# Optimization experiments

Hardware: AMD Instinct MI355X
Metric: run time of the kernel (lower is better)

Reference implementation:

```python
import jax, jax.numpy as jnp
import numpy as np

D_MODEL = 1024
N_HEADS = 16
ALPHA = 0.7
C_PARAM = 5
CUTOFF = C_PARAM // 2 + 1  # 3
LN_EPS = 1e-12
B, S = 4, 2048


def setup_inputs() -> dict:
    key = jax.random.key(0)
    ks = jax.random.split(key, 10)
    d = D_MODEL
    scale = 1.0 / np.sqrt(d)
    return {
        "input_tensor": jax.random.normal(ks[0], (B, S, d), dtype=jnp.float32),
        "attention_mask": jnp.ones((1, 1, S, S), dtype=jnp.int32),
        "sqrt_beta": jax.random.normal(ks[1], (1, 1, d), dtype=jnp.float32),
        "ln_gamma": jnp.ones((d,), dtype=jnp.float32),
        "ln_beta": jnp.zeros((d,), dtype=jnp.float32),
        "q_w": jax.random.normal(ks[2], (d, d), dtype=jnp.float32) * scale,
        "q_b": jnp.zeros((d,), dtype=jnp.float32),
        "k_w": jax.random.normal(ks[3], (d, d), dtype=jnp.float32) * scale,
        "k_b": jnp.zeros((d,), dtype=jnp.float32),
        "v_w": jax.random.normal(ks[4], (d, d), dtype=jnp.float32) * scale,
        "v_b": jnp.zeros((d,), dtype=jnp.float32),
    }


def _layer_norm(x, g, b):
    mu = jnp.mean(x, axis=-1, keepdims=True)
    var = jnp.mean(jnp.square(x - mu), axis=-1, keepdims=True)
    return (x - mu) * jax.lax.rsqrt(var + LN_EPS) * g + b


def bsarec_layer(x, mask, sqrt_beta, ln_gamma, ln_beta, q_w, q_b, k_w, k_b, v_w, v_b):
    batch, seq_len, hidden = x.shape
    # ---- FrequencyLayer (DSP branch) ----
    xf = jnp.fft.rfft(x, axis=1, norm='ortho')                 # [B, S//2+1, D]
    freq = jnp.arange(xf.shape[1])[None, :, None]
    low_pass = jnp.fft.irfft(jnp.where(freq < CUTOFF, xf, 0.0), n=seq_len, axis=1, norm='ortho')
    high_pass = x - low_pass
    seq_fft = low_pass + jnp.square(sqrt_beta) * high_pass
    dsp = _layer_norm(seq_fft + x, ln_gamma, ln_beta)          # dropout=0 -> identity
    # ---- MultiHeadAttention (GSP branch) ----
    h, d_k = N_HEADS, hidden // N_HEADS
    def split(t):  # [B,S,D] -> [B,H,S,d_k]
        return t.reshape(batch, seq_len, h, d_k).transpose(0, 2, 1, 3)
    q = split(x @ q_w.T + q_b)
    k = split(x @ k_w.T + k_b)
    v = split(x @ v_w.T + v_b)
    scores = jnp.einsum('bhsd,bhtd->bhst', q, k) / jnp.sqrt(jnp.float32(d_k))
    scores = jnp.where(mask == 0, -jnp.inf, scores)
    scores = scores - jnp.max(scores)                           # global max, as in source
    p = jax.nn.softmax(scores, axis=-1)
    p = jnp.where(jnp.isnan(p), 0.0, p)
    out = jnp.einsum('bhst,bhtd->bhsd', p, v)
    gsp = out.transpose(0, 2, 1, 3).reshape(batch, seq_len, hidden)
    return ALPHA * dsp + (1.0 - ALPHA) * gsp


def reference(input_tensor, attention_mask, sqrt_beta, ln_gamma, ln_beta, q_w, q_b, k_w, k_b, v_w, v_b):
    return bsarec_layer(input_tensor, attention_mask, sqrt_beta, ln_gamma, ln_beta,
                        q_w, q_b, k_w, k_b, v_w, v_b)
```

## Files before the change

### kernel.cpp

```cpp
#include <hip/hip_runtime.h>

#define S_LEN 2048
#define DM 1024
#define NB 4
#define NROWS (NB * S_LEN)
#define NHEADS 16
#define DK 64

typedef __bf16 bf16x8 __attribute__((ext_vector_type(8)));
typedef __bf16 bf16x2 __attribute__((ext_vector_type(2)));
typedef float f32x4 __attribute__((ext_vector_type(4)));
typedef float f32x2 __attribute__((ext_vector_type(2)));
typedef unsigned u32x4 __attribute__((ext_vector_type(4)));

struct __align__(8) us4 { unsigned short x, y, z, w; };

__device__ __forceinline__ unsigned cvt2(float a, float b) {
    f32x2 t; t.x = a; t.y = b;
    bf16x2 h = __builtin_convertvector(t, bf16x2);
    return __builtin_bit_cast(unsigned, h);
}
__device__ __forceinline__ unsigned short f2bf(float f) {
    __bf16 h = (__bf16)f;
    return __builtin_bit_cast(unsigned short, h);
}

__device__ __forceinline__ void gl2lds16(const void* g, void* l) {
    __builtin_amdgcn_global_load_lds(
        (const __attribute__((address_space(1))) unsigned int*)g,
        (__attribute__((address_space(3))) unsigned int*)l, 16, 0, 0);
}

#if __has_builtin(__builtin_amdgcn_exp2f)
#define EXP2F(x) __builtin_amdgcn_exp2f(x)
#else
#define EXP2F(x) exp2f(x)
#endif

__global__ __launch_bounds__(256) void prep(
    const float* __restrict__ x, float* __restrict__ coef,
    unsigned short* __restrict__ xbf, const float* __restrict__ qw,
    const float* __restrict__ kw, const float* __restrict__ vw,
    unsigned short* __restrict__ wbf) {
    int bx = blockIdx.x;
    if (bx >= 512) {
        int idx = ((bx - 512) * 256 + threadIdx.x) * 2;
        int which = idx >> 20, off = idx & 0xFFFFF;
        const float* src = (which == 0) ? qw : ((which == 1) ? kw : vw);
        float2 v = *(const float2*)(&src[off]);
        *(unsigned*)(&wbf[idx]) = cvt2(v.x, v.y);
        return;
    }
    int b = bx >> 7, dc = (bx >> 5) & 3, tc = bx & 31;
    int d = dc * 256 + threadIdx.x;
    __shared__ float tw[4][64];
    if (threadIdx.x < 64) {
        const float omega = 6.283185307179586476925f / (float)S_LEN;
        float sn, cs;
        __sincosf(omega * (float)(tc * 64 + threadIdx.x), &sn, &cs);
        tw[0][threadIdx.x] = sn;
        tw[1][threadIdx.x] = cs;
        tw[2][threadIdx.x] = 2.f * sn * cs;
        tw[3][threadIdx.x] = cs * cs - sn * sn;
    }
    __syncthreads();
    float c0 = 0.f, c1 = 0.f, s1 = 0.f, c2 = 0.f, s2 = 0.f;
    for (int i = 0; i < 64; ++i) {
        int t = tc * 64 + i;
        long idx = (long)(b * S_LEN + t) * DM + d;
        float v = x[idx];
        xbf[idx] = f2bf(v);
        c0 += v;
        c1 += v * tw[1][i];
        s1 += v * tw[0][i];
        c2 += v * tw[3][i];
        s2 += v * tw[2][i];
    }
    int base = b * DM + d;
    atomicAdd(&coef[0 * 4096 + base], c0);
    atomicAdd(&coef[1 * 4096 + base], c1);
    atomicAdd(&coef[2 * 4096 + base], s1);
    atomicAdd(&coef[3 * 4096 + base], c2);
    atomicAdd(&coef[4 * 4096 + base], s2);
}

__global__ __launch_bounds__(256) void dsp_ln(
    const float* __restrict__ x, const float* __restrict__ coef,
    const float* __restrict__ sqrt_beta, const float* __restrict__ gamma,
    const float* __restrict__ beta, const unsigned short* __restrict__ Og,
    float* __restrict__ out) {
    int row = blockIdx.x;
    int b = row >> 11, t = row & (S_LEN - 1);
    int tid = threadIdx.x, lane = tid & 63, wave = tid >> 6;
    const float omega = 6.283185307179586476925f / (float)S_LEN;
    float sn, cs;
    __sincosf(omega * (float)t, &sn, &cs);
    float c2t = cs * cs - sn * sn, s2t = 2.f * sn * cs;
    int d0 = tid * 4;
    long base = (long)row * DM;
    float4 xv = *(const float4*)(&x[base + d0]);
    int cb = b * DM + d0;
    float4 C0 = *(const float4*)(&coef[0 * 4096 + cb]);
    float4 C1 = *(const float4*)(&coef[1 * 4096 + cb]);
    float4 S1 = *(const float4*)(&coef[2 * 4096 + cb]);
    float4 C2 = *(const float4*)(&coef[3 * 4096 + cb]);
    float4 S2 = *(const float4*)(&coef[4 * 4096 + cb]);
    float4 sb = *(const float4*)(&sqrt_beta[d0]);
    const float inv_s = 1.0f / (float)S_LEN;
    float y[4];
#pragma unroll
    for (int i = 0; i < 4; ++i) {
        float c0 = (&C0.x)[i], c1 = (&C1.x)[i], s1 = (&S1.x)[i],
              c2 = (&C2.x)[i], s2 = (&S2.x)[i];
        float lp = (c0 + 2.f * (c1 * cs + s1 * sn) + 2.f * (c2 * c2t + s2 * s2t)) * inv_s;
        float xx = (&xv.x)[i];
        float b2 = (&sb.x)[i];
        b2 = b2 * b2;
        y[i] = xx + lp + b2 * (xx - lp);
    }
    float ssum = y[0] + y[1] + y[2] + y[3];
    float ssq = y[0] * y[0] + y[1] * y[1] + y[2] * y[2] + y[3] * y[3];
#pragma unroll
    for (int m = 1; m < 64; m <<= 1) {
        ssum += __shfl_xor(ssum, m, 64);
        ssq += __shfl_xor(ssq, m, 64);
    }
    __shared__ float red[8];
    if (lane == 0) { red[wave] = ssum; red[4 + wave] = ssq; }
    __syncthreads();
    float S = red[0] + red[1] + red[2] + red[3];
    float SQ = red[4] + red[5] + red[6] + red[7];
    float mu = S * (1.0f / DM);
    float var = SQ * (1.0f / DM) - mu * mu;
    float rstd = rsqrtf(var + 1e-12f);
    float4 g = *(const float4*)(&gamma[d0]);
    float4 be = *(const float4*)(&beta[d0]);
    us4 gv = *(const us4*)(&Og[((long)((b << 4) + (d0 >> 6)) * S_LEN + t) * DK + (d0 & 63)]);
    const unsigned short* gp = (const unsigned short*)&gv;
    float4 o;
#pragma unroll
    for (int i = 0; i < 4; ++i)
        (&o.x)[i] = 0.7f * ((y[i] - mu) * rstd * (&g.x)[i] + (&be.x)[i]) +
                    0.3f * __uint_as_float((unsigned)gp[i] << 16);
    *(float4*)(&out[base + d0]) = o;
}

__global__ __launch_bounds__(256) void gemm_qkv(
    const unsigned short* __restrict__ A, const unsigned short* __restrict__ W,
    const float* __restrict__ qb, const float* __restrict__ kb,
    const float* __restrict__ vb, unsigned short* __restrict__ Qo,
    unsigned short* __restrict__ Ko, unsigned short* __restrict__ Vt_g) {
    const int m0 = blockIdx.y * 128;
    const int n0g = blockIdx.x * 128;
    const int which = n0g >> 10;
    const int n0 = n0g & 1023;
    const int tid = threadIdx.x;
    const int lane = tid & 63, wave = tid >> 6;
    const int wm = wave >> 1, wn = wave & 1;
    const int r = lane & 15, q = lane >> 4;
    __shared__ __align__(16) unsigned short Sm[8192];
    unsigned short* As = Sm;
    unsigned short* Bs = Sm + 4096;
    const int lrow = lane >> 2;
    const int lch = (lane & 3) * 8;
    f32x4 acc[4][4] = {};
    for (int k0 = 0; k0 < DM; k0 += 32) {
        __syncthreads();
#pragma unroll
        for (int e = 0; e < 2; ++e) {
            int blk = e * 4 + wave;
            int row = blk * 16 + lrow;
            gl2lds16(&A[(long)(m0 + row) * DM + k0 + lch], &As[blk * 512 + lane * 8]);
            gl2lds16(&W[(long)(n0g + row) * DM + k0 + lch], &Bs[blk * 512 + lane * 8]);
        }
        __syncthreads();
        bf16x8 af[4], bfr[4];
#pragma unroll
        for (int i = 0; i < 4; ++i) {
            af[i] = *(const bf16x8*)(&As[(wm * 64 + i * 16 + r) * 32 + q * 8]);
            bfr[i] = *(const bf16x8*)(&Bs[(wn * 64 + i * 16 + r) * 32 + q * 8]);
        }
#pragma unroll
        for (int mi = 0; mi < 4; ++mi)
#pragma unroll
            for (int ni = 0; ni < 4; ++ni)
                acc[mi][ni] = __builtin_amdgcn_mfma_f32_16x16x32_bf16(
                    af[mi], bfr[ni], acc[mi][ni], 0, 0, 0);
    }
    const float* bias = (which == 0) ? qb : ((which == 1) ? kb : vb);
    if (which < 2) {
        const float qs = (which == 0) ? 0.18033688011112042f : 1.0f;
        unsigned short* Out = (which == 0) ? Qo : Ko;
#pragma unroll
        for (int p = 0; p < 4; ++p) {
            __syncthreads();
            if (wm == (p >> 1)) {
#pragma unroll
                for (int mi2 = 0; mi2 < 2; ++mi2) {
                    int mi = (p & 1) * 2 + mi2;
                    int rowL = mi2 * 16 + q * 4;
#pragma unroll
                    for (int ni = 0; ni < 4; ++ni) {
                        int col = wn * 64 + ni * 16 + r;
                        float bv = bias[n0 + col];
#pragma unroll
                        for (int reg = 0; reg < 4; ++reg)
                            Sm[(rowL + reg) * 134 + col] = f2bf((acc[mi][ni][reg] + bv) * qs);
                    }
                }
            }
            __syncthreads();
            int rowL = wave * 8 + (lane >> 3);
            int cc = (lane & 7) * 16;
            uint4 w0 = *(const uint4*)(&Sm[rowL * 134 + cc]);
            uint4 w1 = *(const uint4*)(&Sm[rowL * 134 + cc + 8]);
            long gb = (long)(m0 + p * 32 + rowL) * DM + n0 + cc;
            *(uint4*)(&Out[gb]) = w0;
            *(uint4*)(&Out[gb + 8]) = w1;
        }
    } else {
        const int bb = m0 >> 11, sg = m0 & (S_LEN - 1);
#pragma unroll
        for (int p = 0; p < 4; ++p) {
            __syncthreads();
            if (wn == (p >> 1)) {
#pragma unroll
                for (int ni2 = 0; ni2 < 2; ++ni2) {
                    int ni = (p & 1) * 2 + ni2;
                    int colL = ni2 * 16 + r;
                    float bv = bias[n0 + p * 32 + colL];
#pragma unroll
                    for (int mi = 0; mi < 4; ++mi) {
                        int s = wm * 64 + mi * 16 + q * 4;
                        *(unsigned*)(&Sm[colL * 134 + s]) =
                            cvt2(acc[mi][ni][0] + bv, acc[mi][ni][1] + bv);
                        *(unsigned*)(&Sm[colL * 134 + s + 2]) =
                            cvt2(acc[mi][ni][2] + bv, acc[mi][ni][3] + bv);
                    }
                }
            }
            __syncthreads();
            int colL = wave * 8 + (lane >> 3);
            int sc = (lane & 7) * 16;
            uint4 w0 = *(const uint4*)(&Sm[colL * 134 + sc]);
            uint4 w1 = *(const uint4*)(&Sm[colL * 134 + sc + 8]);
            long gb = ((long)bb * DM + n0 + p * 32 + colL) * S_LEN + sg + sc;
            *(uint4*)(&Vt_g[gb]) = w0;
            *(uint4*)(&Vt_g[gb + 8]) = w1;
        }
    }
}

__global__ __launch_bounds__(256, 3) void attn(
    const unsigned short* __restrict__ Q, const unsigned short* __restrict__ K,
    const unsigned short* __restrict__ Vt_g, unsigned short* __restrict__ Og) {
    int bx = blockIdx.x;
    int bh = bx & 63, qt = bx >> 6;
    int b = bh >> 4, h = bh & 15;
    const int tid = threadIdx.x, lane = tid & 63, wave = tid >> 6;
    const int r = lane & 15, q = lane >> 4;
    const int hc = h * DK;
    const int q0 = qt * 128 + wave * 32;

    bf16x8 aq[2][2];
#pragma unroll
    for (int mt = 0; mt < 2; ++mt) {
        long rowQ = (long)(b * S_LEN + q0 + mt * 16 + r) * DM + hc;
        aq[mt][0] = *(const bf16x8*)(&Q[rowQ + q * 8]);
        aq[mt][1] = *(const bf16x8*)(&Q[rowQ + 32 + q * 8]);
    }

    __shared__ __align__(16) unsigned short Ks[2][4096];
    __shared__ __align__(16) unsigned short Vt[2][4096];
    __shared__ float denL[128];

    f32x4 accO[2][4] = {};
    float den[2] = {};

    const int lr = lane >> 3, lc = lane & 7;
    const int cw0 = wave * 2, cw1 = cw0 + 1;
    const int ld0 = cw0 * 512, ld1 = cw1 * 512;
    const int row0 = cw0 * 8 + lr, row1 = cw1 * 8 + lr;
    const int cg0 = lc ^ lr;
    const int cg1 = lc ^ lr ^ 4;
    const unsigned short* kp0 = K + (long)(b * S_LEN + row0) * DM + hc + cg0 * 8;
    const unsigned short* kp1 = K + (long)(b * S_LEN + row1) * DM + hc + cg1 * 8;
    const unsigned short* vp0 = Vt_g + (long)(bh * 64 + row0) * S_LEN + cg0 * 8;
    const unsigned short* vp1 = Vt_g + (long)(bh * 64 + row1) * S_LEN + cg1 * 8;

    const int lo = r & 3, hi = r >> 2;
    const int abase = (hi * 8 + lo) * 64;
    const int ca = (q ^ lo ^ ((hi & 1) << 2)) * 8;
    const int cb2 = ca ^ 32;
    const int va0 = (q ^ (r & 7) ^ (((r >> 3) & 1) << 2)) * 8;
    const int va1 = va0 ^ 32;

    gl2lds16(kp0, &Ks[0][ld0 + lane * 8]);
    gl2lds16(kp1, &Ks[0][ld1 + lane * 8]);
    gl2lds16(vp0, &Vt[0][ld0 + lane * 8]);
    gl2lds16(vp1, &Vt[0][ld1 + lane * 8]);
    kp0 += 64 * DM; kp1 += 64 * DM; vp0 += 64; vp1 += 64;
    asm volatile("s_waitcnt vmcnt(0)" ::: "memory");
    __builtin_amdgcn_s_barrier();

    for (int t = 0; t < 32; ++t) {
        const int cur = t & 1;
        if (t < 31) {
            const int nb = cur ^ 1;
            gl2lds16(kp0, &Ks[nb][ld0 + lane * 8]);
            gl2lds16(kp1, &Ks[nb][ld1 + lane * 8]);
            gl2lds16(vp0, &Vt[nb][ld0 + lane * 8]);
            gl2lds16(vp1, &Vt[nb][ld1 + lane * 8]);
            kp0 += 64 * DM; kp1 += 64 * DM; vp0 += 64; vp1 += 64;
        }
        const unsigned short* Kc = Ks[cur];
        const unsigned short* Vc = Vt[cur];
#pragma unroll
        for (int c = 0; c < 2; ++c) {
            const int cb64 = c * 2048;
            bf16x8 ak00 = *(const bf16x8*)(&Kc[cb64 + abase + ca]);
            bf16x8 ak01 = *(const bf16x8*)(&Kc[cb64 + abase + cb2]);
            bf16x8 ak10 = *(const bf16x8*)(&Kc[cb64 + 256 + abase + cb2]);
            bf16x8 ak11 = *(const bf16x8*)(&Kc[cb64 + 256 + abase + ca]);
            const int va = c ? va1 : va0;
            bf16x8 bv[4];
            bv[0] = *(const bf16x8*)(&Vc[(0 * 16 + r) * 64 + va]);
            bv[1] = *(const bf16x8*)(&Vc[(1 * 16 + r) * 64 + va]);
            bv[2] = *(const bf16x8*)(&Vc[(2 * 16 + r) * 64 + va]);
            bv[3] = *(const bf16x8*)(&Vc[(3 * 16 + r) * 64 + va]);
#pragma unroll
            for (int mt = 0; mt < 2; ++mt) {
                f32x4 sa = {}, sb = {};
                sa = __builtin_amdgcn_mfma_f32_16x16x32_bf16(ak00, aq[mt][0], sa, 0, 0, 0);
                sa = __builtin_amdgcn_mfma_f32_16x16x32_bf16(ak01, aq[mt][1], sa, 0, 0, 0);
                sb = __builtin_amdgcn_mfma_f32_16x16x32_bf16(ak10, aq[mt][0], sb, 0, 0, 0);
                sb = __builtin_amdgcn_mfma_f32_16x16x32_bf16(ak11, aq[mt][1], sb, 0, 0, 0);
                float p0 = EXP2F(sa[0]), p1 = EXP2F(sa[1]);
                float p2 = EXP2F(sa[2]), p3 = EXP2F(sa[3]);
                float p4 = EXP2F(sb[0]), p5 = EXP2F(sb[1]);
                float p6 = EXP2F(sb[2]), p7 = EXP2F(sb[3]);
                den[mt] += ((p0 + p1) + (p2 + p3)) + ((p4 + p5) + (p6 + p7));
                u32x4 wv;
                wv.x = cvt2(p0, p1); wv.y = cvt2(p2, p3);
                wv.z = cvt2(p4, p5); wv.w = cvt2(p6, p7);
                bf16x8 ap = __builtin_bit_cast(bf16x8, wv);
#pragma unroll
                for (int dt = 0; dt < 4; ++dt)
                    accO[mt][dt] = __builtin_amdgcn_mfma_f32_16x16x32_bf16(
                        ap, bv[dt], accO[mt][dt], 0, 0, 0);
            }
        }
        asm volatile("s_waitcnt vmcnt(0)" ::: "memory");
        __builtin_amdgcn_s_barrier();
    }
#pragma unroll
    for (int mt = 0; mt < 2; ++mt) {
        float d = den[mt];
        d += __shfl_xor(d, 16, 64);
        d += __shfl_xor(d, 32, 64);
        if (q == 0) denL[wave * 32 + mt * 16 + r] = d;
    }
#pragma unroll
    for (int mt = 0; mt < 2; ++mt) {
        float4 dv = *(const float4*)(&denL[wave * 32 + mt * 16 + q * 4]);
        float rs[4];
#pragma unroll
        for (int reg = 0; reg < 4; ++reg) rs[reg] = 1.0f / (&dv.x)[reg];
        long obase = (long)bh * S_LEN + q0 + mt * 16 + q * 4;
#pragma unroll
        for (int dt = 0; dt < 4; ++dt) {
            int col = dt * 16 + r;
#pragma unroll
            for (int reg = 0; reg < 4; ++reg)
                Og[(obase + reg) * DK + col] = f2bf(accO[mt][dt][reg] * rs[reg]);
        }
    }
}

extern "C" void kernel_launch(void* const* d_in, const int* in_sizes, int n_in,
                              void* d_out, int out_size, void* d_ws, size_t ws_size,
                              hipStream_t stream) {
    const float* x = (const float*)d_in[0];
    const float* sqrt_beta = (const float*)d_in[2];
    const float* gamma = (const float*)d_in[3];
    const float* beta = (const float*)d_in[4];
    const float* qw = (const float*)d_in[5];
    const float* qb = (const float*)d_in[6];
    const float* kw = (const float*)d_in[7];
    const float* kb = (const float*)d_in[8];
    const float* vw = (const float*)d_in[9];
    const float* vb = (const float*)d_in[10];
    float* out = (float*)d_out;

    char* ws = (char*)d_ws;
    float* coef = (float*)ws;
    unsigned short* xbf = (unsigned short*)(ws + 81920);
    unsigned short* wbf = (unsigned short*)(ws + 81920 + 16777216);
    unsigned short* Qb = (unsigned short*)(ws + 81920 + 16777216 + 6291456);
    unsigned short* Kb = Qb + (long)NROWS * DM;
    unsigned short* Vt_g = Kb + (long)NROWS * DM;
    unsigned short* Og = xbf;

    hipMemsetAsync(coef, 0, 5 * 4096 * sizeof(float), stream);
    prep<<<6656, 256, 0, stream>>>(x, coef, xbf, qw, kw, vw, wbf);
    dim3 ggrid(3 * DM / 128, NROWS / 128);
    gemm_qkv<<<ggrid, 256, 0, stream>>>(xbf, wbf, qb, kb, vb, Qb, Kb, Vt_g);
    attn<<<NB * NHEADS * (S_LEN / 128), 256, 0, stream>>>(Qb, Kb, Vt_g, Og);
    dsp_ln<<<NROWS, 256, 0, stream>>>(x, coef, sqrt_beta, gamma, beta, Og, out);
}
```

Before: 300.3 us.

## Triple-buffer K/V tiles in attention and raise priority around MFMA section

Turns the K/V shared-memory staging in the attention kernel from double to triple buffering. Two tiles are prefetched ahead and the loop waits with vmcnt(4) instead of vmcnt(0), so one tile load can stay in flight across the barrier. It also raises wave priority with s_setprio during the MFMA compute section. LDS use per block grows from about 32KB to 48KB, which may lower occupancy.

```diff
diff --git a/kernel.cpp b/kernel.cpp
--- a/kernel.cpp
+++ b/kernel.cpp
@@ -270,8 +270,8 @@
         aq[mt][1] = *(const bf16x8*)(&Q[rowQ + 32 + q * 8]);
     }
 
-    __shared__ __align__(16) unsigned short Ks[2][4096];
-    __shared__ __align__(16) unsigned short Vt[2][4096];
+    __shared__ __align__(16) unsigned short Ks[3][4096];
+    __shared__ __align__(16) unsigned short Vt[3][4096];
     __shared__ float denL[128];
 
     f32x4 accO[2][4] = {};
@@ -295,26 +295,29 @@
     const int va0 = (q ^ (r & 7) ^ (((r >> 3) & 1) << 2)) * 8;
     const int va1 = va0 ^ 32;
 
-    gl2lds16(kp0, &Ks[0][ld0 + lane * 8]);
-    gl2lds16(kp1, &Ks[0][ld1 + lane * 8]);
-    gl2lds16(vp0, &Vt[0][ld0 + lane * 8]);
-    gl2lds16(vp1, &Vt[0][ld1 + lane * 8]);
-    kp0 += 64 * DM; kp1 += 64 * DM; vp0 += 64; vp1 += 64;
-    asm volatile("s_waitcnt vmcnt(0)" ::: "memory");
+#define STAGE(buf)                                    \
+    do {                                              \
+        gl2lds16(kp0, &Ks[buf][ld0 + lane * 8]);      \
+        gl2lds16(kp1, &Ks[buf][ld1 + lane * 8]);      \
+        gl2lds16(vp0, &Vt[buf][ld0 + lane * 8]);      \
+        gl2lds16(vp1, &Vt[buf][ld1 + lane * 8]);      \
+        kp0 += 64 * DM; kp1 += 64 * DM; vp0 += 64; vp1 += 64; \
+    } while (0)
+
+    STAGE(0);
+    STAGE(1);
+    asm volatile("s_waitcnt vmcnt(4)" ::: "memory");
     __builtin_amdgcn_s_barrier();
 
+    int cur = 0, nb = 2;
     for (int t = 0; t < 32; ++t) {
-        const int cur = t & 1;
-        if (t < 31) {
-            const int nb = cur ^ 1;
-            gl2lds16(kp0, &Ks[nb][ld0 + lane * 8]);
-            gl2lds16(kp1, &Ks[nb][ld1 + lane * 8]);
-            gl2lds16(vp0, &Vt[nb][ld0 + lane * 8]);
-            gl2lds16(vp1, &Vt[nb][ld1 + lane * 8]);
-            kp0 += 64 * DM; kp1 += 64 * DM; vp0 += 64; vp1 += 64;
+        if (t < 30) {
+            STAGE(nb);
+            nb = (nb == 2) ? 0 : nb + 1;
         }
         const unsigned short* Kc = Ks[cur];
         const unsigned short* Vc = Vt[cur];
+        __builtin_amdgcn_s_setprio(1);
 #pragma unroll
         for (int c = 0; c < 2; ++c) {
             const int cb64 = c * 2048;
@@ -350,9 +353,18 @@
                         ap, bv[dt], accO[mt][dt], 0, 0, 0);
             }
         }
-        asm volatile("s_waitcnt vmcnt(0)" ::: "memory");
+        __builtin_amdgcn_s_setprio(0);
+        if (t == 31) break;
+        if (t < 30) {
+            asm volatile("s_waitcnt vmcnt(4)" ::: "memory");
+        } else {
+            asm volatile("s_waitcnt vmcnt(0)" ::: "memory");
+        }
         __builtin_amdgcn_s_barrier();
-    }
+        cur = (cur == 2) ? 0 : cur + 1;
+    }
+#undef STAGE
+
 #pragma unroll
     for (int mt = 0; mt < 2; ++mt) {
         float d = den[mt];
```

Result: faster. 292.6 us (-2.6%).
